# Kernel optimization log

Measured on AMD Instinct MI355X. Metric: run time of the kernel, lower is better.

## Reference

```python
import jax, jax.numpy as jnp
import numpy as np

GT_POSITIVE_THRESHOLD = 3.0  # pixels, from config['gt_positive_threshold']


def setup_inputs() -> dict:
    key = jax.random.key(0)
    k0, k1, k2 = jax.random.split(key, 3)
    B, N0, N1 = 8, 2048, 2048
    W, H = 640.0, 480.0
    scale = jnp.array([W, H], dtype=jnp.float32)
    kpts0 = jax.random.uniform(k0, (B, N0, 2), dtype=jnp.float32) * scale
    kpts1 = jax.random.uniform(k1, (B, N1, 2), dtype=jnp.float32) * scale
    # near-identity homography per pair (small perturbation keeps points in-frame)
    transformation = (jnp.eye(3, dtype=jnp.float32)[None]
                      + 0.001 * jax.random.normal(k2, (B, 3, 3), dtype=jnp.float32))
    return {"kpts0": kpts0, "kpts1": kpts1, "transformation": transformation}


def _reproject_keypoints(kpts, H):
    # kpts: [B,N,2], H: [B,3,3] homography. Homogeneous projection.
    ones = jnp.ones(kpts.shape[:-1] + (1,), dtype=kpts.dtype)
    pts_h = jnp.concatenate([kpts, ones], axis=-1)           # [B,N,3]
    proj = jnp.einsum('bij,bnj->bni', H, pts_h)              # [B,N,3]
    return proj[..., :2] / (proj[..., 2:3] + 1e-8)


def _cdist(a, b):
    # a: [B,N0,2], b: [B,N1,2] -> [B,N0,N1] Euclidean distances
    a2 = jnp.sum(a * a, axis=-1)                             # [B,N0]
    b2 = jnp.sum(b * b, axis=-1)                             # [B,N1]
    ab = jnp.einsum('bnd,bmd->bnm', a, b)                    # [B,N0,N1]
    d2 = a2[:, :, None] + b2[:, None, :] - 2.0 * ab
    return jnp.sqrt(jnp.maximum(d2, 0.0))


def reference(kpts0, kpts1, transformation):
    B, N0, _ = kpts0.shape
    N1 = kpts1.shape[1]
    kpts0_t = _reproject_keypoints(kpts0, transformation)
    err = _cdist(kpts0_t, kpts1)                             # [B,N0,N1]

    min_dist0 = jnp.min(err, axis=2)                         # [B,N0]
    gt_matches0 = jnp.argmin(err, axis=2).astype(jnp.int32)  # [B,N0]
    gt_matches1 = jnp.argmin(err, axis=1).astype(jnp.int32)  # [B,N1]

    # cross-check: kpts1's best match of kpts0's best match must be the kpt itself
    back = jnp.take_along_axis(gt_matches1, gt_matches0, axis=1)  # [B,N0]
    idx0 = jnp.arange(N0, dtype=jnp.int32)[None, :]
    inconsistent = (back != idx0) | (min_dist0 > GT_POSITIVE_THRESHOLD)
    gt_matches0 = jnp.where(inconsistent, -1, gt_matches0)

    # rebuild inverse map: gt_matches1[b, gt_matches0[b,i]] = i for valid i
    valid = gt_matches0 != -1
    tgt = jnp.where(valid, gt_matches0, N1)                  # N1 is out-of-range -> dropped
    src = jnp.broadcast_to(idx0, (B, N0))
    gt_matches1_out = jnp.full((B, N1), -1, dtype=jnp.int32)
    gt_matches1_out = gt_matches1_out.at[jnp.arange(B)[:, None], tgt].set(src, mode='drop')

    return gt_matches0, gt_matches1_out, min_dist0
```

## Files before the change

### kernel.cpp

```cpp
#include <hip/hip_runtime.h>


#define SPN 2048
#define SPT 16384

__device__ __forceinline__ void sp_reproject(const float* __restrict__ T, int b,
                                             float x, float y,
                                             float& X, float& Y, float& S) {
  const float* H = T + b * 9;
  float p0 = __fadd_rn(__fadd_rn(__fmul_rn(H[0], x), __fmul_rn(H[1], y)), H[2]);
  float p1 = __fadd_rn(__fadd_rn(__fmul_rn(H[3], x), __fmul_rn(H[4], y)), H[5]);
  float p2 = __fadd_rn(__fadd_rn(__fmul_rn(H[6], x), __fmul_rn(H[7], y)), H[8]);
  float den = __fadd_rn(p2, 1e-8f);
  X = __fdiv_rn(p0, den);
  Y = __fdiv_rn(p1, den);
  S = __fadd_rn(__fmul_rn(X, X), __fmul_rn(Y, Y));
}

__global__ __launch_bounds__(256) void sp_prep(
    const float2* __restrict__ k0, const float2* __restrict__ k1,
    const float* __restrict__ T, float4* __restrict__ q0, float4* __restrict__ q1) {
  int t = blockIdx.x * 256 + threadIdx.x;
  if (t < SPT) {
    float2 p = k0[t];
    float X, Y, S;
    sp_reproject(T, t >> 11, p.x, p.y, X, Y, S);
    q0[t] = make_float4(X, Y, S, 0.0f);
  } else {
    int u = t - SPT;
    float2 p = k1[u];
    float S = __fadd_rn(__fmul_rn(p.x, p.x), __fmul_rn(p.y, p.y));
    q1[u] = make_float4(p.x, p.y, S, 0.0f);
  }
}

__global__ __launch_bounds__(256) void SuperPointMatchesGenerator_56925496541369_kernel(
    const float4* __restrict__ q0, const float4* __restrict__ q1,
    unsigned short* __restrict__ gt0p, unsigned short* __restrict__ gt1,
    float* __restrict__ out_mind) {
  const bool m1 = blockIdx.x >= SPN;
  const int base = (m1 ? blockIdx.x - SPN : blockIdx.x) * 8;
  const int b = base >> 11, cb = b << 11;
  const float4* __restrict__ qr = m1 ? q1 : q0;
  const float4* __restrict__ qc = m1 ? q0 : q1;

  float rx[8], ry[8], rs[8], bv[8];
  int bi[8];
#pragma unroll
  for (int r = 0; r < 8; r++) {
    float4 v = qr[base + r];
    rx[r] = v.x; ry[r] = v.y; rs[r] = v.z;
    bv[r] = INFINITY; bi[r] = 0;
  }

#pragma unroll 4
  for (int c = threadIdx.x; c < SPN; c += 256) {
    float4 v = qc[cb + c];
#pragma unroll
    for (int r = 0; r < 8; r++) {
      float ab = __fadd_rn(__fmul_rn(rx[r], v.x), __fmul_rn(ry[r], v.y));
      float d2 = __fsub_rn(__fadd_rn(rs[r], v.z), __fmul_rn(2.0f, ab));
      float dm = fmaxf(d2, 0.0f);
      if (dm < bv[r]) { bv[r] = dm; bi[r] = c; }
    }
  }

  unsigned long long key[8];
#pragma unroll
  for (int r = 0; r < 8; r++)
    key[r] = ((unsigned long long)__float_as_uint(bv[r]) << 32) | (unsigned)bi[r];
#pragma unroll
  for (int off = 32; off > 0; off >>= 1) {
#pragma unroll
    for (int r = 0; r < 8; r++) {
      unsigned long long o = __shfl_down(key[r], off);
      if (o < key[r]) key[r] = o;
    }
  }
  __shared__ unsigned long long part[4][8];
  if ((threadIdx.x & 63) == 0) {
    int w = threadIdx.x >> 6;
#pragma unroll
    for (int r = 0; r < 8; r++) part[w][r] = key[r];
  }
  __syncthreads();
  if (threadIdx.x < 8) {
    int r = threadIdx.x;
    unsigned long long k = part[0][r];
#pragma unroll
    for (int w = 1; w < 4; w++)
      if (part[w][r] < k) k = part[w][r];
    int idx = (int)(k & 0x7ffu);
    if (!m1) {
      float dm = __uint_as_float((unsigned)(k >> 32));
      float e = __fsqrt_rn(dm);
      unsigned short pk = (unsigned short)idx;
      if (e > 3.0f) pk |= 0x8000u;
      gt0p[base + r] = pk;
      out_mind[base + r] = e;
    } else {
      gt1[base + r] = (unsigned short)idx;
    }
  }
}

__global__ __launch_bounds__(256) void SuperPointMatchesGenerator_56925496541369_final(
    const unsigned short* __restrict__ gt0p, const unsigned short* __restrict__ gt1,
    float* __restrict__ out) {
  int t = blockIdx.x * 256 + threadIdx.x;
  if (t >= SPT) return;
  int b = t >> 11, i = t & 2047, cb = b << 11;

  unsigned short p0 = gt0p[t];
  int m0 = p0 & 0x7ff;
  bool ok0 = ((p0 & 0x8000u) == 0) && ((int)gt1[cb + m0] == i);
  out[t] = ok0 ? (float)m0 : -1.0f;

  int istar = gt1[t];
  unsigned short ps = gt0p[cb + istar];
  bool ok1 = (((int)(ps & 0x7ff)) == i) && ((ps & 0x8000u) == 0);
  out[SPT + t] = ok1 ? (float)istar : -1.0f;
}

__global__ __launch_bounds__(256) void sp_fallback_main(
    const float2* __restrict__ k0, const float2* __restrict__ k1,
    const float* __restrict__ T, unsigned short* __restrict__ gt0p,
    unsigned short* __restrict__ gt1, float* __restrict__ out_mind) {
  const bool mode1 = blockIdx.x >= SPN;
  const int base = (mode1 ? blockIdx.x - SPN : blockIdx.x) * 8;
  const int b = base >> 11, cb = b << 11;
  float rx[8], ry[8], rs[8], bv[8];
  int bi[8];
#pragma unroll
  for (int r = 0; r < 8; r++) { bv[r] = INFINITY; bi[r] = 0; }
  if (!mode1) {
#pragma unroll
    for (int r = 0; r < 8; r++) {
      float2 p = k0[base + r];
      sp_reproject(T, b, p.x, p.y, rx[r], ry[r], rs[r]);
    }
    for (int c = threadIdx.x; c < SPN; c += 256) {
      float2 p = k1[cb + c];
      float b2 = __fadd_rn(__fmul_rn(p.x, p.x), __fmul_rn(p.y, p.y));
#pragma unroll
      for (int r = 0; r < 8; r++) {
        float ab = __fadd_rn(__fmul_rn(rx[r], p.x), __fmul_rn(ry[r], p.y));
        float d2 = __fsub_rn(__fadd_rn(rs[r], b2), __fmul_rn(2.0f, ab));
        float dm = fmaxf(d2, 0.0f);
        if (dm < bv[r]) { bv[r] = dm; bi[r] = c; }
      }
    }
  } else {
#pragma unroll
    for (int r = 0; r < 8; r++) {
      float2 p = k1[base + r];
      rx[r] = p.x; ry[r] = p.y;
      rs[r] = __fadd_rn(__fmul_rn(p.x, p.x), __fmul_rn(p.y, p.y));
    }
    for (int c = threadIdx.x; c < SPN; c += 256) {
      float2 p = k0[cb + c];
      float cx, cy, a2;
      sp_reproject(T, b, p.x, p.y, cx, cy, a2);
#pragma unroll
      for (int r = 0; r < 8; r++) {
        float ab = __fadd_rn(__fmul_rn(rx[r], cx), __fmul_rn(ry[r], cy));
        float d2 = __fsub_rn(__fadd_rn(a2, rs[r]), __fmul_rn(2.0f, ab));
        float dm = fmaxf(d2, 0.0f);
        if (dm < bv[r]) { bv[r] = dm; bi[r] = c; }
      }
    }
  }
  unsigned long long key[8];
#pragma unroll
  for (int r = 0; r < 8; r++)
    key[r] = ((unsigned long long)__float_as_uint(bv[r]) << 32) | (unsigned)bi[r];
#pragma unroll
  for (int off = 32; off > 0; off >>= 1) {
#pragma unroll
    for (int r = 0; r < 8; r++) {
      unsigned long long o = __shfl_down(key[r], off);
      if (o < key[r]) key[r] = o;
    }
  }
  __shared__ unsigned long long part[4][8];
  if ((threadIdx.x & 63) == 0) {
    int w = threadIdx.x >> 6;
#pragma unroll
    for (int r = 0; r < 8; r++) part[w][r] = key[r];
  }
  __syncthreads();
  if (threadIdx.x < 8) {
    int r = threadIdx.x;
    unsigned long long k = part[0][r];
#pragma unroll
    for (int w = 1; w < 4; w++)
      if (part[w][r] < k) k = part[w][r];
    int idx = (int)(k & 0x7ffu);
    if (!mode1) {
      float e = __fsqrt_rn(__uint_as_float((unsigned)(k >> 32)));
      unsigned short pk = (unsigned short)idx;
      if (e > 3.0f) pk |= 0x8000u;
      gt0p[base + r] = pk;
      out_mind[base + r] = e;
    } else {
      gt1[base + r] = (unsigned short)idx;
    }
  }
}

extern "C" void kernel_launch(void* const* d_in, const int* in_sizes, int n_in,
                              void* d_out, int out_size, void* d_ws, size_t ws_size,
                              hipStream_t stream) {
  (void)in_sizes; (void)n_in; (void)out_size;
  const float2* k0 = (const float2*)d_in[0];
  const float2* k1 = (const float2*)d_in[1];
  const float* T   = (const float*)d_in[2];
  float* out = (float*)d_out;

  const size_t need = (size_t)2 * SPT * sizeof(float4) + (size_t)2 * SPT * sizeof(unsigned short);
  if (ws_size >= need) {
    float4* q0 = (float4*)d_ws;
    float4* q1 = q0 + SPT;
    unsigned short* gt0p = (unsigned short*)(q1 + SPT);
    unsigned short* gt1  = gt0p + SPT;
    sp_prep<<<2 * SPT / 256, 256, 0, stream>>>(k0, k1, T, q0, q1);
    SuperPointMatchesGenerator_56925496541369_kernel<<<2 * SPN, 256, 0, stream>>>(
        q0, q1, gt0p, gt1, out + 2 * SPT);
    SuperPointMatchesGenerator_56925496541369_final<<<SPT / 256, 256, 0, stream>>>(
        gt0p, gt1, out);
  } else {
    unsigned short* gt0p = (unsigned short*)d_ws;
    unsigned short* gt1  = gt0p + SPT;
    sp_fallback_main<<<2 * SPN, 256, 0, stream>>>(k0, k1, T, gt0p, gt1, out + 2 * SPT);
    SuperPointMatchesGenerator_56925496541369_final<<<SPT / 256, 256, 0, stream>>>(
        gt0p, gt1, out);
  }
}
```

Baseline: 84.09 us.

## Compute row and column argmin in one pass with atomicMin column keys

The separate row and column argmin passes over the distance matrix are merged into one. Each block handles 16 rows, tracks a per-column best row within the block, and merges it into a global 64-bit key array with atomicMin. This halves the distance evaluations and doubles rows per block. It also pre-doubles the row coordinates so the factor-of-two multiply is dropped, which could change rounding in rare cases. It adds one global 64-bit atomic per column per block, 128 contending blocks per column.

```diff
diff --git a/kernel.cpp b/kernel.cpp
--- a/kernel.cpp
+++ b/kernel.cpp
@@ -3,6 +3,7 @@
 
 #define SPN 2048
 #define SPT 16384
+#define RPB 16
 
 __device__ __forceinline__ void sp_reproject(const float* __restrict__ T, int b,
                                              float x, float y,
@@ -19,13 +20,15 @@
 
 __global__ __launch_bounds__(256) void sp_prep(
     const float2* __restrict__ k0, const float2* __restrict__ k1,
-    const float* __restrict__ T, float4* __restrict__ q0, float4* __restrict__ q1) {
+    const float* __restrict__ T, float4* __restrict__ q0, float4* __restrict__ q1,
+    unsigned long long* __restrict__ colkeys) {
   int t = blockIdx.x * 256 + threadIdx.x;
   if (t < SPT) {
     float2 p = k0[t];
     float X, Y, S;
     sp_reproject(T, t >> 11, p.x, p.y, X, Y, S);
     q0[t] = make_float4(X, Y, S, 0.0f);
+    colkeys[t] = ~0ull;
   } else {
     int u = t - SPT;
     float2 p = k1[u];
@@ -36,93 +39,95 @@
 
 __global__ __launch_bounds__(256) void SuperPointMatchesGenerator_56925496541369_kernel(
     const float4* __restrict__ q0, const float4* __restrict__ q1,
-    unsigned short* __restrict__ gt0p, unsigned short* __restrict__ gt1,
+    unsigned short* __restrict__ gt0p, unsigned long long* __restrict__ colkeys,
     float* __restrict__ out_mind) {
-  const bool m1 = blockIdx.x >= SPN;
-  const int base = (m1 ? blockIdx.x - SPN : blockIdx.x) * 8;
+  const int base = blockIdx.x * RPB;
   const int b = base >> 11, cb = b << 11;
-  const float4* __restrict__ qr = m1 ? q1 : q0;
-  const float4* __restrict__ qc = m1 ? q0 : q1;
-
-  float rx[8], ry[8], rs[8], bv[8];
-  int bi[8];
-#pragma unroll
-  for (int r = 0; r < 8; r++) {
-    float4 v = qr[base + r];
-    rx[r] = v.x; ry[r] = v.y; rs[r] = v.z;
+  const int base_ib = base & 2047;
+
+  float rx2[RPB], ry2[RPB], rs[RPB], bv[RPB];
+  int bi[RPB];
+#pragma unroll
+  for (int r = 0; r < RPB; r++) {
+    float4 v = q0[base + r];
+    rx2[r] = __fadd_rn(v.x, v.x);
+    ry2[r] = __fadd_rn(v.y, v.y);
+    rs[r] = v.z;
     bv[r] = INFINITY; bi[r] = 0;
   }
 
-#pragma unroll 4
+#pragma unroll 2
   for (int c = threadIdx.x; c < SPN; c += 256) {
-    float4 v = qc[cb + c];
-#pragma unroll
-    for (int r = 0; r < 8; r++) {
-      float ab = __fadd_rn(__fmul_rn(rx[r], v.x), __fmul_rn(ry[r], v.y));
-      float d2 = __fsub_rn(__fadd_rn(rs[r], v.z), __fmul_rn(2.0f, ab));
+    float4 v = q1[cb + c];
+    float cbv = INFINITY;
+    int cbr = 0;
+#pragma unroll
+    for (int r = 0; r < RPB; r++) {
+      float ab2 = __fadd_rn(__fmul_rn(rx2[r], v.x), __fmul_rn(ry2[r], v.y));
+      float d2 = __fsub_rn(__fadd_rn(rs[r], v.z), ab2);
       float dm = fmaxf(d2, 0.0f);
       if (dm < bv[r]) { bv[r] = dm; bi[r] = c; }
-    }
-  }
-
-  unsigned long long key[8];
-#pragma unroll
-  for (int r = 0; r < 8; r++)
+      if (dm < cbv)   { cbv = dm; cbr = r; }
+    }
+    unsigned long long ck =
+        ((unsigned long long)__float_as_uint(cbv) << 32) | (unsigned)(base_ib + cbr);
+    atomicMin(&colkeys[cb + c], ck);
+  }
+
+  unsigned long long key[RPB];
+#pragma unroll
+  for (int r = 0; r < RPB; r++)
     key[r] = ((unsigned long long)__float_as_uint(bv[r]) << 32) | (unsigned)bi[r];
 #pragma unroll
   for (int off = 32; off > 0; off >>= 1) {
 #pragma unroll
-    for (int r = 0; r < 8; r++) {
+    for (int r = 0; r < RPB; r++) {
       unsigned long long o = __shfl_down(key[r], off);
       if (o < key[r]) key[r] = o;
     }
   }
-  __shared__ unsigned long long part[4][8];
+  __shared__ unsigned long long part[4][RPB];
   if ((threadIdx.x & 63) == 0) {
     int w = threadIdx.x >> 6;
 #pragma unroll
-    for (int r = 0; r < 8; r++) part[w][r] = key[r];
+    for (int r = 0; r < RPB; r++) part[w][r] = key[r];
   }
   __syncthreads();
-  if (threadIdx.x < 8) {
+  if (threadIdx.x < RPB) {
     int r = threadIdx.x;
     unsigned long long k = part[0][r];
 #pragma unroll
     for (int w = 1; w < 4; w++)
       if (part[w][r] < k) k = part[w][r];
     int idx = (int)(k & 0x7ffu);
-    if (!m1) {
-      float dm = __uint_as_float((unsigned)(k >> 32));
-      float e = __fsqrt_rn(dm);
-      unsigned short pk = (unsigned short)idx;
-      if (e > 3.0f) pk |= 0x8000u;
-      gt0p[base + r] = pk;
-      out_mind[base + r] = e;
-    } else {
-      gt1[base + r] = (unsigned short)idx;
-    }
+    float e = __fsqrt_rn(__uint_as_float((unsigned)(k >> 32)));
+    unsigned short pk = (unsigned short)idx;
+    if (e > 3.0f) pk |= 0x8000u;
+    gt0p[base + r] = pk;
+    out_mind[base + r] = e;
   }
 }
 
 __global__ __launch_bounds__(256) void SuperPointMatchesGenerator_56925496541369_final(
-    const unsigned short* __restrict__ gt0p, const unsigned short* __restrict__ gt1,
-    float* __restrict__ out) {
+    const unsigned short* __restrict__ gt0p,
+    const unsigned long long* __restrict__ colkeys, float* __restrict__ out) {
   int t = blockIdx.x * 256 + threadIdx.x;
   if (t >= SPT) return;
   int b = t >> 11, i = t & 2047, cb = b << 11;
 
   unsigned short p0 = gt0p[t];
   int m0 = p0 & 0x7ff;
-  bool ok0 = ((p0 & 0x8000u) == 0) && ((int)gt1[cb + m0] == i);
+  int back = (int)(colkeys[cb + m0] & 0x7ffu);
+  bool ok0 = ((p0 & 0x8000u) == 0) && (back == i);
   out[t] = ok0 ? (float)m0 : -1.0f;
 
-  int istar = gt1[t];
+  int istar = (int)(colkeys[t] & 0x7ffu);
   unsigned short ps = gt0p[cb + istar];
   bool ok1 = (((int)(ps & 0x7ff)) == i) && ((ps & 0x8000u) == 0);
   out[SPT + t] = ok1 ? (float)istar : -1.0f;
 }
 
-__global__ __launch_bounds__(256) void sp_fallback_main(
+__global__ __launch_bounds__(256) void sp_fb_main(
     const float2* __restrict__ k0, const float2* __restrict__ k1,
     const float* __restrict__ T, unsigned short* __restrict__ gt0p,
     unsigned short* __restrict__ gt1, float* __restrict__ out_mind) {
@@ -208,6 +213,22 @@
   }
 }
 
+__global__ __launch_bounds__(256) void sp_fb_final(
+    const unsigned short* __restrict__ gt0p, const unsigned short* __restrict__ gt1,
+    float* __restrict__ out) {
+  int t = blockIdx.x * 256 + threadIdx.x;
+  if (t >= SPT) return;
+  int b = t >> 11, i = t & 2047, cb = b << 11;
+  unsigned short p0 = gt0p[t];
+  int m0 = p0 & 0x7ff;
+  bool ok0 = ((p0 & 0x8000u) == 0) && ((int)gt1[cb + m0] == i);
+  out[t] = ok0 ? (float)m0 : -1.0f;
+  int istar = gt1[t];
+  unsigned short ps = gt0p[cb + istar];
+  bool ok1 = (((int)(ps & 0x7ff)) == i) && ((ps & 0x8000u) == 0);
+  out[SPT + t] = ok1 ? (float)istar : -1.0f;
+}
+
 extern "C" void kernel_launch(void* const* d_in, const int* in_sizes, int n_in,
                               void* d_out, int out_size, void* d_ws, size_t ws_size,
                               hipStream_t stream) {
@@ -217,22 +238,23 @@
   const float* T   = (const float*)d_in[2];
   float* out = (float*)d_out;
 
-  const size_t need = (size_t)2 * SPT * sizeof(float4) + (size_t)2 * SPT * sizeof(unsigned short);
+  const size_t need = (size_t)2 * SPT * sizeof(float4)
+                    + (size_t)SPT * sizeof(unsigned long long)
+                    + (size_t)SPT * sizeof(unsigned short);
   if (ws_size >= need) {
     float4* q0 = (float4*)d_ws;
     float4* q1 = q0 + SPT;
-    unsigned short* gt0p = (unsigned short*)(q1 + SPT);
-    unsigned short* gt1  = gt0p + SPT;
-    sp_prep<<<2 * SPT / 256, 256, 0, stream>>>(k0, k1, T, q0, q1);
-    SuperPointMatchesGenerator_56925496541369_kernel<<<2 * SPN, 256, 0, stream>>>(
-        q0, q1, gt0p, gt1, out + 2 * SPT);
+    unsigned long long* colkeys = (unsigned long long*)(q1 + SPT);
+    unsigned short* gt0p = (unsigned short*)(colkeys + SPT);
+    sp_prep<<<2 * SPT / 256, 256, 0, stream>>>(k0, k1, T, q0, q1, colkeys);
+    SuperPointMatchesGenerator_56925496541369_kernel<<<SPT / RPB, 256, 0, stream>>>(
+        q0, q1, gt0p, colkeys, out + 2 * SPT);
     SuperPointMatchesGenerator_56925496541369_final<<<SPT / 256, 256, 0, stream>>>(
-        gt0p, gt1, out);
+        gt0p, colkeys, out);
   } else {
     unsigned short* gt0p = (unsigned short*)d_ws;
     unsigned short* gt1  = gt0p + SPT;
-    sp_fallback_main<<<2 * SPN, 256, 0, stream>>>(k0, k1, T, gt0p, gt1, out + 2 * SPT);
-    SuperPointMatchesGenerator_56925496541369_final<<<SPT / 256, 256, 0, stream>>>(
-        gt0p, gt1, out);
-  }
-}
+    sp_fb_main<<<2 * SPN, 256, 0, stream>>>(k0, k1, T, gt0p, gt1, out + 2 * SPT);
+    sp_fb_final<<<SPT / 256, 256, 0, stream>>>(gt0p, gt1, out);
+  }
+}
```

Result: slower. 89.99 us (+7.0%).
